# Performance work log

Measured on AMD Instinct MI355X. Metric: run time of the kernel, lower is better.

Reference implementation:

```python
import jax, jax.numpy as jnp
import numpy as np
import math

N = 4096
D = 256
H = 8
DH = D // H
E_RAND = 131072
EPS = 1e-5


def _layernorm(x, g, b):
    mu = jnp.mean(x, axis=-1, keepdims=True)
    var = jnp.mean((x - mu) ** 2, axis=-1, keepdims=True)
    return (x - mu) * jax.lax.rsqrt(var + EPS) * g + b


def setup_inputs() -> dict:
    key = jax.random.key(0)
    ks = jax.random.split(key, 16)
    s = 1.0 / math.sqrt(D)
    x = jax.random.normal(ks[0], (N, D), dtype=jnp.float32)
    src = jax.random.randint(ks[1], (E_RAND,), 0, N)
    dst = jax.random.randint(ks[2], (E_RAND,), 0, N)
    loop = jnp.arange(N)
    edge_index = jnp.stack([jnp.concatenate([src, loop]),
                            jnp.concatenate([dst, loop])]).astype(jnp.int64)
    def lin(k):
        return jax.random.normal(k, (D, D), dtype=jnp.float32) * s
    return {
        "x": x,
        "edge_index": edge_index,
        "Wq": lin(ks[3]), "bq": jnp.zeros((D,), jnp.float32),
        "Wk": lin(ks[4]), "bk": jnp.zeros((D,), jnp.float32),
        "Wv": lin(ks[5]), "bv": jnp.zeros((D,), jnp.float32),
        "Wo": lin(ks[6]), "bo": jnp.zeros((D,), jnp.float32),
        "g1": jnp.ones((D,), jnp.float32), "b1": jnp.zeros((D,), jnp.float32),
        "g2": jnp.ones((D,), jnp.float32), "b2": jnp.zeros((D,), jnp.float32),
        "Wm1": jax.random.normal(ks[7], (D, 2 * D), jnp.float32) * s,
        "bm1": jnp.zeros((2 * D,), jnp.float32),
        "Wm2": jax.random.normal(ks[8], (2 * D, D), jnp.float32) * (1.0 / math.sqrt(2 * D)),
        "bm2": jnp.zeros((D,), jnp.float32),
    }


def reference(x, edge_index, Wq, bq, Wk, bk, Wv, bv, Wo, bo,
              g1, b1, g2, b2, Wm1, bm1, Wm2, bm2):
    scale = 1.0 / math.sqrt(DH)
    h = _layernorm(x, g1, b1)
    # [N, D] -> [H, N, DH]
    q = (h @ Wq + bq).reshape(N, H, DH).transpose(1, 0, 2)
    k = (h @ Wk + bk).reshape(N, H, DH).transpose(1, 0, 2)
    v = (h @ Wv + bv).reshape(N, H, DH).transpose(1, 0, 2)
    att = jnp.einsum('hnd,hmd->hnm', q, k) * scale  # [H, N, N]
    # mask: True everywhere except edges (edge positions are attended)
    mask = jnp.ones((N, N), dtype=bool).at[edge_index[0], edge_index[1]].set(False)
    att = jnp.where(mask[None, :, :], -jnp.inf, att)
    att = jax.nn.softmax(att, axis=-1)
    y = jnp.einsum('hnm,hmd->hnd', att, v)  # [H, N, DH]
    y = y.transpose(1, 0, 2).reshape(N, D)
    x = x + (y @ Wo + bo)
    h2 = _layernorm(x, g2, b2)
    x = x + (jax.nn.gelu(h2 @ Wm1 + bm1, approximate=False) @ Wm2 + bm2)
    return x
```

## Files before the change

kernel.cpp:

```cpp
#include <hip/hip_runtime.h>
#include <hip/hip_bf16.h>

#define N_NODES 4096
#define D_MODEL 256
#define NWORDS 128
#define CAP 128

typedef __attribute__((ext_vector_type(8))) short short8;
typedef __attribute__((ext_vector_type(4))) float f32x4;

__device__ __forceinline__ unsigned short f2b(float f) {
    unsigned u = __float_as_uint(f);
    return (unsigned short)((u + 0x7FFFu + ((u >> 16) & 1u)) >> 16);
}
__device__ __forceinline__ float b2f(unsigned short u) {
    return __uint_as_float((unsigned)u << 16);
}

__global__ __launch_bounds__(256) void prep_kernel(const float* __restrict__ Wq,
        const float* __restrict__ Wk, const float* __restrict__ Wv,
        const float* __restrict__ Wo, const float* __restrict__ Wm1,
        const float* __restrict__ Wm2, unsigned short* __restrict__ wbf,
        uint4* __restrict__ bitmap, const int* __restrict__ ei,
        int* __restrict__ flag, const float* __restrict__ x,
        const float* __restrict__ g1, const float* __restrict__ b1,
        unsigned short* __restrict__ h) {
    int b = blockIdx.x, t = threadIdx.x;
    if (b < 2048) {
        int e = b * 256 + t;
        const float* W; int base, K, M;
        if (e < 262144) {
            int r = e >> 16;
            W = (r == 0) ? Wq : (r == 1) ? Wk : (r == 2) ? Wv : Wo;
            base = r << 16; K = 256; M = 256;
        } else if (e < 393216) { W = Wm1; base = 262144; K = 256; M = 512; }
        else                   { W = Wm2; base = 393216; K = 512; M = 256; }
        int i = e - base;
        int m = i / K, k = i - m * K;
        wbf[e] = f2b(W[k * M + m]);
    } else if (b < 2560) {
        bitmap[(size_t)(b - 2048) * 256 + t] = uint4{0, 0, 0, 0};
    } else if (b == 2560) {
        if (t == 0) {
            int is64 = 1;
            for (int i = 1; i < 128; i += 2)
                if (ei[i] != 0) { is64 = 0; break; }
            *flag = is64;
        }
    } else {
        int row = b - 2561;
        float v = x[row * D_MODEL + t];
        __shared__ float red[4];
        float s = v;
        #pragma unroll
        for (int off = 32; off; off >>= 1) s += __shfl_down(s, off, 64);
        if ((t & 63) == 0) red[t >> 6] = s;
        __syncthreads();
        float mu = (red[0] + red[1] + red[2] + red[3]) * (1.0f / 256.0f);
        __syncthreads();
        float d = v - mu;
        float s2 = d * d;
        #pragma unroll
        for (int off = 32; off; off >>= 1) s2 += __shfl_down(s2, off, 64);
        if ((t & 63) == 0) red[t >> 6] = s2;
        __syncthreads();
        float var = (red[0] + red[1] + red[2] + red[3]) * (1.0f / 256.0f);
        h[row * D_MODEL + t] = f2b(d * rsqrtf(var + 1e-5f) * g1[t] + b1[t]);
    }
}

template <int K, int MODE, bool LNA, bool STATS>
__global__ __launch_bounds__(512) void gemm_bf16(const unsigned short* __restrict__ A,
        const float* __restrict__ Af, const float* __restrict__ psum,
        const float* __restrict__ psum2, const float* __restrict__ lng,
        const float* __restrict__ lnb, const unsigned short* __restrict__ BT,
        const float* __restrict__ bias, const float* __restrict__ bias_k,
        const float* __restrict__ bias_v, const float* __restrict__ R,
        float* __restrict__ Cf, unsigned short* __restrict__ Cb,
        unsigned short* __restrict__ Ck, unsigned short* __restrict__ Cv,
        float* __restrict__ opsum, float* __restrict__ opsum2, int M,
        const int* __restrict__ ei, int E, const int* __restrict__ flag,
        unsigned* __restrict__ bitmap, int nadj) {
    int tid = threadIdx.x;
    if (MODE == 3 && (int)blockIdx.x < nadj) {
        int e = (int)blockIdx.x * 512 + tid;
        if (e < E) {
            int n, m;
            if (*flag) { n = ei[2 * e]; m = ei[2 * (E + e)]; }
            else       { n = ei[e];     m = ei[E + e]; }
            atomicOr(&bitmap[n * NWORDS + (m >> 5)], 1u << (m & 31));
        }
        return;
    }
    __shared__ unsigned short Asm[64][72];
    __shared__ unsigned short Bsm[64][72];
    __shared__ float psA[64][2], psA2[64][2];
    __shared__ float muS[64], invS[64];

    int bx2  = (MODE == 3) ? ((int)blockIdx.x - nadj) : 0;
    int brow = (MODE == 3) ? ((bx2 & 63) << 6) : ((int)blockIdx.x << 6);
    int by   = (MODE == 3) ? (bx2 >> 6) : (int)blockIdx.y;
    int bcol = by << 6;
    int wid = tid >> 6, lane = tid & 63;
    int wr = wid >> 1, wc = wid & 1;
    int l15 = lane & 15, lhi = lane >> 4;
    int r0 = tid >> 3, c0 = (tid & 7) << 3;

    float mu_r = 0.f, inv_r = 0.f;
    if (LNA) {
        if (tid < 64) {
            float4 s4 = ((const float4*)psum)[brow + tid];
            float4 q4 = ((const float4*)psum2)[brow + tid];
            float S  = s4.x + s4.y + s4.z + s4.w;
            float S2 = q4.x + q4.y + q4.z + q4.w;
            float mu = S * (1.0f / 256.0f);
            muS[tid] = mu;
            invS[tid] = rsqrtf(S2 * (1.0f / 256.0f) - mu * mu + 1e-5f);
        }
        __syncthreads();
        mu_r = muS[r0]; inv_r = invS[r0];
    }

    const unsigned short* Bp = BT + (size_t)(bcol + r0) * K + c0;
    f32x4 acc[2] = {};
    short8 areg;
    float4 xa, xb, ga, gb, ba, bb;
    if (LNA) {
        const float* Xp = Af + (size_t)(brow + r0) * 256 + c0;
        xa = *(const float4*)(Xp);
        xb = *(const float4*)(Xp + 4);
        ga = *(const float4*)(lng + c0); gb = *(const float4*)(lng + c0 + 4);
        ba = *(const float4*)(lnb + c0); bb = *(const float4*)(lnb + c0 + 4);
    } else {
        areg = *(const short8*)(A + (size_t)(brow + r0) * K + c0);
    }
    short8 breg = *(const short8*)(Bp);

    #pragma unroll
    for (int k0 = 0; k0 < K; k0 += 64) {
        if (LNA) {
            float xv[8] = {xa.x, xa.y, xa.z, xa.w, xb.x, xb.y, xb.z, xb.w};
            float gv[8] = {ga.x, ga.y, ga.z, ga.w, gb.x, gb.y, gb.z, gb.w};
            float bv[8] = {ba.x, ba.y, ba.z, ba.w, bb.x, bb.y, bb.z, bb.w};
            short8 o;
            #pragma unroll
            for (int j = 0; j < 8; ++j)
                o[j] = (short)f2b((xv[j] - mu_r) * inv_r * gv[j] + bv[j]);
            *(short8*)&Asm[r0][c0] = o;
        } else {
            *(short8*)&Asm[r0][c0] = areg;
        }
        *(short8*)&Bsm[r0][c0] = breg;
        __syncthreads();
        if (k0 + 64 < K) {
            if (LNA) {
                const float* Xp = Af + (size_t)(brow + r0) * 256 + k0 + 64 + c0;
                xa = *(const float4*)(Xp);
                xb = *(const float4*)(Xp + 4);
                ga = *(const float4*)(lng + k0 + 64 + c0);
                gb = *(const float4*)(lng + k0 + 64 + c0 + 4);
                ba = *(const float4*)(lnb + k0 + 64 + c0);
                bb = *(const float4*)(lnb + k0 + 64 + c0 + 4);
            } else {
                areg = *(const short8*)(A + (size_t)(brow + r0) * K + k0 + 64 + c0);
            }
            breg = *(const short8*)(Bp + k0 + 64);
        }
        #pragma unroll
        for (int ks = 0; ks < 2; ++ks) {
            int kc = ks * 32 + lhi * 8;
            short8 a_0 = *(const short8*)&Asm[wr * 16 + l15][kc];
            short8 b_0 = *(const short8*)&Bsm[wc * 32 + l15][kc];
            short8 b_1 = *(const short8*)&Bsm[wc * 32 + 16 + l15][kc];
            acc[0] = __builtin_amdgcn_mfma_f32_16x16x32_bf16(a_0, b_0, acc[0], 0, 0, 0);
            acc[1] = __builtin_amdgcn_mfma_f32_16x16x32_bf16(a_0, b_1, acc[1], 0, 0, 0);
        }
        __syncthreads();
    }

    float cs[2][4];
    #pragma unroll
    for (int sn = 0; sn < 2; ++sn) {
        int col = bcol + wc * 32 + sn * 16 + l15;
        float bs;
        if (MODE == 3)
            bs = (col < 256) ? bias[col]
               : (col < 512) ? bias_k[col - 256] : bias_v[col - 512];
        else
            bs = bias[col];
        #pragma unroll
        for (int r = 0; r < 4; ++r) {
            int row = brow + wr * 16 + lhi * 4 + r;
            float c = acc[sn][r] + bs;
            if (MODE == 1) {
                c = 0.5f * c * (1.0f + erff(c * 0.70710678118654752f));
                Cb[(size_t)row * M + col] = f2b(c);
            } else if (MODE == 2) {
                c += R[(size_t)row * M + col];
                Cf[(size_t)row * M + col] = c;
            } else if (MODE == 3) {
                int part = col >> 8, cc = col & 255;
                unsigned short* dst = (part == 0) ? Cb : (part == 1) ? Ck : Cv;
                dst[(((size_t)(cc >> 5) * N_NODES + row) << 5) + (cc & 31)] = f2b(c);
            } else {
                Cb[(size_t)row * M + col] = f2b(c);
            }
            if (STATS) cs[sn][r] = c;
        }
    }
    if (STATS) {
        #pragma unroll
        for (int r = 0; r < 4; ++r) {
            float s  = cs[0][r] + cs[1][r];
            float s2 = cs[0][r] * cs[0][r] + cs[1][r] * cs[1][r];
            #pragma unroll
            for (int off = 1; off < 16; off <<= 1) {
                s  += __shfl_xor(s, off, 64);
                s2 += __shfl_xor(s2, off, 64);
            }
            if (l15 == 0) {
                int rl = wr * 16 + lhi * 4 + r;
                psA[rl][wc] = s; psA2[rl][wc] = s2;
            }
        }
        __syncthreads();
        if (tid < 64) {
            opsum [(size_t)(brow + tid) * 4 + by] = psA[tid][0] + psA[tid][1];
            opsum2[(size_t)(brow + tid) * 4 + by] = psA2[tid][0] + psA2[tid][1];
        }
    }
}

__global__ __launch_bounds__(256) void attn_kernel(const unsigned short* __restrict__ qh,
        const unsigned short* __restrict__ kh, const unsigned short* __restrict__ vh,
        const unsigned* __restrict__ bitmap, unsigned short* __restrict__ y) {
    int bid = blockIdx.x, tid = threadIdx.x;
    int h = bid & 7, oct = bid >> 3;
    int g = tid >> 5, lane = tid & 31;
    int n = oct * 8 + g;
    __shared__ int sIdx[8][CAP];
    __shared__ unsigned short Vst[8][64][36];

    const unsigned short* qp = qh + (((size_t)h * N_NODES + n) << 5);
    float qreg[32];
    #pragma unroll
    for (int i = 0; i < 4; ++i) {
        short8 q8 = *(const short8*)(qp + i * 8);
        #pragma unroll
        for (int j = 0; j < 8; ++j) qreg[i * 8 + j] = b2f((unsigned short)q8[j]);
    }

    uint4 w4 = ((const uint4*)(bitmap + (size_t)n * NWORDS))[lane];
    unsigned words[4] = {w4.x, w4.y, w4.z, w4.w};
    int pc = __popc(w4.x) + __popc(w4.y) + __popc(w4.z) + __popc(w4.w);
    int pre = pc;
    #pragma unroll
    for (int off = 1; off < 32; off <<= 1) {
        int u = __shfl_up(pre, off, 32);
        if (lane >= off) pre += u;
    }
    int c = __shfl(pre, 31, 32);
    int off = pre - pc;
    #pragma unroll
    for (int i = 0; i < 4; ++i) {
        unsigned word = words[i];
        int wbase = ((lane << 2) + i) << 5;
        while (word) {
            int bit = __ffs(word) - 1;
            word &= word - 1;
            if (off < CAP) sIdx[g][off] = wbase + bit;
            ++off;
        }
    }
    c = min(c, CAP);
    for (int i = c + lane; i < 64; i += 32) sIdx[g][i] = 0;
    __syncthreads();

    int idx_a = sIdx[g][lane], idx_b = sIdx[g][lane + 32];
    const size_t hb = (size_t)h * N_NODES << 5;

    const unsigned short* va = vh + hb + ((size_t)idx_a << 5);
    const unsigned short* vb = vh + hb + ((size_t)idx_b << 5);
    short8 va0 = *(const short8*)(va);      short8 va1 = *(const short8*)(va + 8);
    short8 va2 = *(const short8*)(va + 16); short8 va3 = *(const short8*)(va + 24);
    short8 vb0 = *(const short8*)(vb);      short8 vb1 = *(const short8*)(vb + 8);
    short8 vb2 = *(const short8*)(vb + 16); short8 vb3 = *(const short8*)(vb + 24);

    const unsigned short* ka = kh + hb + ((size_t)idx_a << 5);
    const unsigned short* kb = kh + hb + ((size_t)idx_b << 5);
    short8 ka0 = *(const short8*)(ka);      short8 ka1 = *(const short8*)(ka + 8);
    short8 ka2 = *(const short8*)(ka + 16); short8 ka3 = *(const short8*)(ka + 24);
    short8 kb0 = *(const short8*)(kb);      short8 kb1 = *(const short8*)(kb + 8);
    short8 kb2 = *(const short8*)(kb + 16); short8 kb3 = *(const short8*)(kb + 24);

    *(short8*)&Vst[g][lane][0]       = va0;
    *(short8*)&Vst[g][lane][8]       = va1;
    *(short8*)&Vst[g][lane][16]      = va2;
    *(short8*)&Vst[g][lane][24]      = va3;
    *(short8*)&Vst[g][lane + 32][0]  = vb0;
    *(short8*)&Vst[g][lane + 32][8]  = vb1;
    *(short8*)&Vst[g][lane + 32][16] = vb2;
    *(short8*)&Vst[g][lane + 32][24] = vb3;

    float da0 = 0.f, da1 = 0.f, db0 = 0.f, db1 = 0.f;
    #pragma unroll
    for (int e = 0; e < 8; ++e) {
        da0 = fmaf(qreg[e],      b2f((unsigned short)ka0[e]), da0);
        da1 = fmaf(qreg[8 + e],  b2f((unsigned short)ka1[e]), da1);
        da0 = fmaf(qreg[16 + e], b2f((unsigned short)ka2[e]), da0);
        da1 = fmaf(qreg[24 + e], b2f((unsigned short)ka3[e]), da1);
        db0 = fmaf(qreg[e],      b2f((unsigned short)kb0[e]), db0);
        db1 = fmaf(qreg[8 + e],  b2f((unsigned short)kb1[e]), db1);
        db0 = fmaf(qreg[16 + e], b2f((unsigned short)kb2[e]), db0);
        db1 = fmaf(qreg[24 + e], b2f((unsigned short)kb3[e]), db1);
    }
    const float sc = 0.17677669529663687f;
    float s_a = (lane < c)      ? (da0 + da1) * sc : -INFINITY;
    float s_b = (lane + 32 < c) ? (db0 + db1) * sc : -INFINITY;

    float bm = fmaxf(s_a, s_b);
    #pragma unroll
    for (int o2 = 16; o2; o2 >>= 1) bm = fmaxf(bm, __shfl_xor(bm, o2, 32));
    float p_a = (lane < c)      ? __expf(s_a - bm) : 0.0f;
    float p_b = (lane + 32 < c) ? __expf(s_b - bm) : 0.0f;
    float S = p_a + p_b;
    #pragma unroll
    for (int o2 = 16; o2; o2 >>= 1) S += __shfl_xor(S, o2, 32);

    float acc0 = 0.f, acc1 = 0.f;
    #pragma unroll
    for (int jj = 0; jj < 32; ++jj) {
        float pa = __shfl(p_a, jj, 32);
        float pb = __shfl(p_b, jj, 32);
        acc0 = fmaf(pa, b2f(Vst[g][jj][lane]), acc0);
        acc1 = fmaf(pb, b2f(Vst[g][jj + 32][lane]), acc1);
    }
    float acc = acc0 + acc1;

    if (c > 64) {
        float m_run = bm;
        for (int b0 = 64; b0 < c; b0 += 32) {
            int j = b0 + lane;
            float s = -INFINITY;
            if (j < c) {
                const unsigned short* kp = kh + hb + ((size_t)sIdx[g][j] << 5);
                float d = 0.0f;
                #pragma unroll
                for (int i = 0; i < 4; ++i) {
                    short8 k8 = *(const short8*)(kp + i * 8);
                    #pragma unroll
                    for (int e = 0; e < 8; ++e)
                        d = fmaf(qreg[i * 8 + e], b2f((unsigned short)k8[e]), d);
                }
                s = d * sc;
            }
            float bm2 = s;
            #pragma unroll
            for (int o2 = 16; o2; o2 >>= 1) bm2 = fmaxf(bm2, __shfl_xor(bm2, o2, 32));
            float newM = fmaxf(m_run, bm2);
            float p = (j < c) ? __expf(s - newM) : 0.0f;
            float bs = p;
            #pragma unroll
            for (int o2 = 16; o2; o2 >>= 1) bs += __shfl_xor(bs, o2, 32);
            float scale = __expf(m_run - newM);
            S = S * scale + bs;
            acc *= scale;
            int lim = min(32, c - b0);
            const unsigned short* vbase = vh + hb + lane;
            for (int jj = 0; jj < lim; ++jj) {
                float pj = __shfl(p, jj, 32);
                acc = fmaf(pj, b2f(vbase[(size_t)sIdx[g][b0 + jj] << 5]), acc);
            }
            m_run = newM;
        }
    }
    y[(size_t)n * 256 + h * 32 + lane] = f2b(acc / S);
}

extern "C" void kernel_launch(void* const* d_in, const int* in_sizes, int n_in,
                              void* d_out, int out_size, void* d_ws, size_t ws_size,
                              hipStream_t stream) {
    const float* x   = (const float*)d_in[0];
    const int*   ei  = (const int*)d_in[1];
    const float* Wq  = (const float*)d_in[2];  const float* bq  = (const float*)d_in[3];
    const float* Wk  = (const float*)d_in[4];  const float* bk  = (const float*)d_in[5];
    const float* Wv  = (const float*)d_in[6];  const float* bv  = (const float*)d_in[7];
    const float* Wo  = (const float*)d_in[8];  const float* bo  = (const float*)d_in[9];
    const float* g1  = (const float*)d_in[10]; const float* b1  = (const float*)d_in[11];
    const float* g2  = (const float*)d_in[12]; const float* b2  = (const float*)d_in[13];
    const float* Wm1 = (const float*)d_in[14]; const float* bm1 = (const float*)d_in[15];
    const float* Wm2 = (const float*)d_in[16]; const float* bm2 = (const float*)d_in[17];
    float* out = (float*)d_out;
    int E = in_sizes[1] / 2;
    int nadj = (E + 511) / 512;

    char* WS = (char*)d_ws;
    const size_t MB = 1u << 20;
    unsigned*       bitmap = (unsigned*)WS;
    int*            flag   = (int*)(WS + 2 * MB);
    float*          psum   = (float*)(WS + 2 * MB + 4096);
    float*          psum2  = (float*)(WS + 2 * MB + 4096 + 65536);
    unsigned short* wbf    = (unsigned short*)(WS + 3 * MB);
    unsigned short* y      = (unsigned short*)(WS + 4 * MB);
    float*          x1     = (float*)(WS + 6 * MB);
    unsigned short* m1     = (unsigned short*)(WS + 10 * MB);
    unsigned short* h      = (unsigned short*)(WS + 14 * MB);
    unsigned short* qh     = (unsigned short*)(WS + 16 * MB);
    unsigned short* kh     = (unsigned short*)(WS + 18 * MB);
    unsigned short* vh     = (unsigned short*)(WS + 20 * MB);

    const unsigned short* WTqkv = wbf;
    const unsigned short* WTo   = wbf + 196608;
    const unsigned short* WTm1  = wbf + 262144;
    const unsigned short* WTm2  = wbf + 393216;

    prep_kernel<<<6657, 256, 0, stream>>>(Wq, Wk, Wv, Wo, Wm1, Wm2, wbf,
                                          (uint4*)bitmap, ei, flag, x, g1, b1, h);
    gemm_bf16<256, 3, false, false><<<nadj + 768, 512, 0, stream>>>(h, nullptr,
            nullptr, nullptr, nullptr, nullptr, WTqkv, bq, bk, bv, nullptr,
            nullptr, qh, kh, vh, nullptr, nullptr, 768, ei, E, flag, bitmap, nadj);
    attn_kernel<<<N_NODES, 256, 0, stream>>>(qh, kh, vh, bitmap, y);
    gemm_bf16<256, 2, false, true><<<dim3(64, 4), 512, 0, stream>>>(y, nullptr,
            nullptr, nullptr, nullptr, nullptr, WTo, bo, nullptr, nullptr, x,
            x1, nullptr, nullptr, nullptr, psum, psum2, 256, nullptr, 0, nullptr, nullptr, 0);
    gemm_bf16<256, 1, true, false><<<dim3(64, 8), 512, 0, stream>>>(nullptr, x1,
            psum, psum2, g2, b2, WTm1, bm1, nullptr, nullptr, nullptr,
            nullptr, m1, nullptr, nullptr, nullptr, nullptr, 512, nullptr, 0, nullptr, nullptr, 0);
    gemm_bf16<512, 2, false, false><<<dim3(64, 4), 512, 0, stream>>>(m1, nullptr,
            nullptr, nullptr, nullptr, nullptr, WTm2, bm2, nullptr, nullptr, x1,
            out, nullptr, nullptr, nullptr, nullptr, nullptr, 256, nullptr, 0, nullptr, nullptr, 0);
}
```

Before: 75.08 us.

## Use LDS transpose reads and shared prob array for the attention PV product

Reorganizes the staged V tile in shared memory into a layout readable with ds_read_b64_tr_b16 transpose loads. Probabilities are written to a shared array and read back as float4, which replaces 64 cross-lane shuffles per row in the P·V accumulation. CAP is reduced from 128 to 96 to shrink LDS use. The change relies on inline asm, manual waitcnt and a scheduling barrier, and the tight manual layout carries a correctness risk if the transpose semantics or the offsets are wrong.

Result: faster. 70.30 us (-6.4%).

```diff
diff --git a/kernel.cpp b/kernel.cpp
--- a/kernel.cpp
+++ b/kernel.cpp
@@ -4,9 +4,10 @@
 #define N_NODES 4096
 #define D_MODEL 256
 #define NWORDS 128
-#define CAP 128
+#define CAP 96
 
 typedef __attribute__((ext_vector_type(8))) short short8;
+typedef __attribute__((ext_vector_type(4))) short short4v;
 typedef __attribute__((ext_vector_type(4))) float f32x4;
 
 __device__ __forceinline__ unsigned short f2b(float f) {
@@ -231,6 +232,16 @@
     }
 }
 
+#define TRLOAD(dst_, OFF_) \
+    asm volatile("ds_read_b64_tr_b16 %0, %1 offset:" #OFF_ \
+                 : "=v"(dst_) : "v"(trbase))
+#define PVSTEP(tv_, b_) { \
+    float4 pv = *(const float4*)&pArr[g][4 * (b_)]; \
+    acc = fmaf(pv.x, b2f((unsigned short)tv_[0]), acc); \
+    acc = fmaf(pv.y, b2f((unsigned short)tv_[1]), acc); \
+    acc = fmaf(pv.z, b2f((unsigned short)tv_[2]), acc); \
+    acc = fmaf(pv.w, b2f((unsigned short)tv_[3]), acc); }
+
 __global__ __launch_bounds__(256) void attn_kernel(const unsigned short* __restrict__ qh,
         const unsigned short* __restrict__ kh, const unsigned short* __restrict__ vh,
         const unsigned* __restrict__ bitmap, unsigned short* __restrict__ y) {
@@ -239,7 +250,8 @@
     int g = tid >> 5, lane = tid & 31;
     int n = oct * 8 + g;
     __shared__ int sIdx[8][CAP];
-    __shared__ unsigned short Vst[8][64][36];
+    __shared__ unsigned short Vst[8][2176];
+    __shared__ float pArr[8][64];
 
     const unsigned short* qp = qh + (((size_t)h * N_NODES + n) << 5);
     float qreg[32];
@@ -293,14 +305,18 @@
     short8 kb0 = *(const short8*)(kb);      short8 kb1 = *(const short8*)(kb + 8);
     short8 kb2 = *(const short8*)(kb + 16); short8 kb3 = *(const short8*)(kb + 24);
 
-    *(short8*)&Vst[g][lane][0]       = va0;
-    *(short8*)&Vst[g][lane][8]       = va1;
-    *(short8*)&Vst[g][lane][16]      = va2;
-    *(short8*)&Vst[g][lane][24]      = va3;
-    *(short8*)&Vst[g][lane + 32][0]  = vb0;
-    *(short8*)&Vst[g][lane + 32][8]  = vb1;
-    *(short8*)&Vst[g][lane + 32][16] = vb2;
-    *(short8*)&Vst[g][lane + 32][24] = vb3;
+    {
+        unsigned short* vr = &Vst[g][(lane >> 2) * 136 + (lane & 3) * 16];
+        *(short8*)(vr + 0)  = va0;
+        *(short8*)(vr + 8)  = va1;
+        *(short8*)(vr + 64) = va2;
+        *(short8*)(vr + 72) = va3;
+        unsigned short* vr2 = vr + 8 * 136;
+        *(short8*)(vr2 + 0)  = vb0;
+        *(short8*)(vr2 + 8)  = vb1;
+        *(short8*)(vr2 + 64) = vb2;
+        *(short8*)(vr2 + 72) = vb3;
+    }
 
     float da0 = 0.f, da1 = 0.f, db0 = 0.f, db1 = 0.f;
     #pragma unroll
@@ -326,16 +342,25 @@
     float S = p_a + p_b;
     #pragma unroll
     for (int o2 = 16; o2; o2 >>= 1) S += __shfl_xor(S, o2, 32);
-
-    float acc0 = 0.f, acc1 = 0.f;
-    #pragma unroll
-    for (int jj = 0; jj < 32; ++jj) {
-        float pa = __shfl(p_a, jj, 32);
-        float pb = __shfl(p_b, jj, 32);
-        acc0 = fmaf(pa, b2f(Vst[g][jj][lane]), acc0);
-        acc1 = fmaf(pb, b2f(Vst[g][jj + 32][lane]), acc1);
-    }
-    float acc = acc0 + acc1;
+    pArr[g][lane] = p_a;
+    pArr[g][lane + 32] = p_b;
+
+    unsigned trbase = (unsigned)(uintptr_t)(&Vst[g][0])
+                    + ((unsigned)(lane >> 4) << 7) + ((unsigned)(lane & 15) << 3);
+    asm volatile("s_waitcnt lgkmcnt(0)" ::: "memory");
+    short4v t0, t1, t2, t3, t4, t5, t6, t7, t8, t9, t10, t11, t12, t13, t14, t15;
+    TRLOAD(t0, 0);     TRLOAD(t1, 272);  TRLOAD(t2, 544);  TRLOAD(t3, 816);
+    TRLOAD(t4, 1088);  TRLOAD(t5, 1360); TRLOAD(t6, 1632); TRLOAD(t7, 1904);
+    TRLOAD(t8, 2176);  TRLOAD(t9, 2448); TRLOAD(t10, 2720); TRLOAD(t11, 2992);
+    TRLOAD(t12, 3264); TRLOAD(t13, 3536); TRLOAD(t14, 3808); TRLOAD(t15, 4080);
+    asm volatile("s_waitcnt lgkmcnt(0)" ::: "memory");
+    __builtin_amdgcn_sched_barrier(0);
+
+    float acc = 0.0f;
+    PVSTEP(t0, 0)   PVSTEP(t1, 1)   PVSTEP(t2, 2)   PVSTEP(t3, 3)
+    PVSTEP(t4, 4)   PVSTEP(t5, 5)   PVSTEP(t6, 6)   PVSTEP(t7, 7)
+    PVSTEP(t8, 8)   PVSTEP(t9, 9)   PVSTEP(t10, 10) PVSTEP(t11, 11)
+    PVSTEP(t12, 12) PVSTEP(t13, 13) PVSTEP(t14, 14) PVSTEP(t15, 15)
 
     if (c > 64) {
         float m_run = bm;
```
